# Performance work log

Hardware: AMD Instinct MI355X
Metric: run time of the kernel (lower is better)

## Reference

```python
import jax, jax.numpy as jnp
import numpy as np

N_NODES = 50000
N_EDGES = 800000
NUM_GRAPHS = 64
D_IN = 128
D_HID = 128
D_EMB = 128
D_PRED = 256
D_OUT = 1
BN_EPS = 1e-5


def gcn_conv(x, W, b, src, dst, n_nodes):
    # PyG GCNConv: add self-loops, sym-normalize, aggregate, then bias.
    h = x @ W  # [N, d_out]
    # in-degree with self-loops
    deg = jax.ops.segment_sum(jnp.ones((src.shape[0],), h.dtype), dst,
                              num_segments=n_nodes) + 1.0
    inv_sqrt = 1.0 / jnp.sqrt(deg)  # [N]
    norm = inv_sqrt[src] * inv_sqrt[dst]  # [E]
    msg = h[src] * norm[:, None]  # [E, d_out] gather + scale
    agg = jax.ops.segment_sum(msg, dst, num_segments=n_nodes)
    # self-loop contribution: norm_ii = 1/deg_i
    agg = agg + h / deg[:, None]
    return agg + b


def batch_norm(h, gamma, beta):
    # BatchNorm1d in training mode: batch stats, biased variance
    mean = jnp.mean(h, axis=0)
    var = jnp.mean(jnp.square(h - mean), axis=0)
    return (h - mean) / jnp.sqrt(var + BN_EPS) * gamma + beta


def setup_inputs() -> dict:
    key = jax.random.key(0)
    ks = jax.random.split(key, 12)
    x = jax.random.normal(ks[0], (N_NODES, D_IN), dtype=jnp.float32)
    edge_index = jax.random.randint(ks[1], (2, N_EDGES), 0, N_NODES, dtype=jnp.int32)
    batch = jnp.sort(jax.random.randint(ks[2], (N_NODES,), 0, NUM_GRAPHS, dtype=jnp.int32))
    s1 = 1.0 / np.sqrt(D_IN)
    s2 = 1.0 / np.sqrt(D_HID)
    s3 = 1.0 / np.sqrt(D_EMB)
    s4 = 1.0 / np.sqrt(D_PRED)
    return {
        "x": x,
        "edge_index": edge_index,
        "batch": batch,
        "W1": jax.random.uniform(ks[3], (D_IN, D_HID), jnp.float32, -s1, s1),
        "b1": jnp.zeros((D_HID,), jnp.float32),
        "g1": jnp.ones((D_HID,), jnp.float32),
        "be1": jnp.zeros((D_HID,), jnp.float32),
        "W2": jax.random.uniform(ks[4], (D_HID, D_EMB), jnp.float32, -s2, s2),
        "b2": jnp.zeros((D_EMB,), jnp.float32),
        "g2": jnp.ones((D_EMB,), jnp.float32),
        "be2": jnp.zeros((D_EMB,), jnp.float32),
        "Wp1": jax.random.uniform(ks[5], (D_EMB, D_PRED), jnp.float32, -s3, s3),
        "bp1": jax.random.uniform(ks[6], (D_PRED,), jnp.float32, -s3, s3),
        "Wp2": jax.random.uniform(ks[7], (D_PRED, D_OUT), jnp.float32, -s4, s4),
        "bp2": jax.random.uniform(ks[8], (D_OUT,), jnp.float32, -s4, s4),
    }


def reference(x, edge_index, batch, W1, b1, g1, be1, W2, b2, g2, be2, Wp1, bp1, Wp2, bp2):
    src, dst = edge_index[0], edge_index[1]
    h = gcn_conv(x, W1, b1, src, dst, N_NODES)
    h = batch_norm(jax.nn.relu(h), g1, be1)
    h = gcn_conv(h, W2, b2, src, dst, N_NODES)
    h = batch_norm(jax.nn.relu(h), g2, be2)
    # global max pool per graph
    pooled = jax.ops.segment_max(h, batch, num_segments=NUM_GRAPHS)  # [G, D_EMB]
    # predictor MLP (Dropout is identity in eval)
    z = jax.nn.relu(pooled @ Wp1 + bp1)
    return z @ Wp2 + bp2
```

## Files before the change

kernel.cpp:

```cpp
#include <hip/hip_runtime.h>

#define NN 50000
#define NE 800000
#define NG 64
#define D 128
#define DP 256
#define BN_EPS 1e-5f
#define NSLOT 32
#define NB 196

typedef unsigned short bf16;
typedef __attribute__((ext_vector_type(8))) short s16x8;
typedef __attribute__((ext_vector_type(4))) float f32x4;

__device__ __forceinline__ float bf2f(unsigned h16) {
  unsigned u = (h16 & 0xffffu) << 16; float f; __builtin_memcpy(&f, &u, 4); return f;
}
__device__ __forceinline__ bf16 f2bf(float f) {
  unsigned u; __builtin_memcpy(&u, &f, 4);
  return (bf16)((u + 0x7FFFu + ((u >> 16) & 1u)) >> 16);
}
__device__ __forceinline__ unsigned packbf2(float a, float b) {
  return (unsigned)f2bf(a) | ((unsigned)f2bf(b) << 16);
}
__device__ __forceinline__ s16x8 u4cast(uint4 v) {
  s16x8 r; __builtin_memcpy(&r, &v, 16); return r;
}

__global__ void k_detect(const unsigned short* __restrict__ x, int* __restrict__ flag) {
  if (threadIdx.x == 0) {
    int good = 0;
    for (int i = 0; i < 64; ++i) {
      float v = bf2f(x[2 * i]);
      float a = fabsf(v);
      if (v == 0.0f || (a > 1e-30f && a < 32.0f)) good++;
    }
    flag[0] = (good >= 56) ? 1 : 0;
    flag[1] = 1;
  }
}

struct CvtArgs {
  const void* s[12];
  float* d[12];
  int n[12];
};

__global__ __launch_bounds__(256) void k_cvt(CvtArgs a, const int* __restrict__ flag) {
  int t = blockIdx.x;
  int mode = flag[0];
  const void* sp = a.s[t];
  float* dp = a.d[t];
  int n = a.n[t];
  if (mode) {
    const unsigned short* s = (const unsigned short*)sp;
    for (int i = threadIdx.x; i < n; i += 256) dp[i] = bf2f(s[i]);
  } else {
    const float* s = (const float*)sp;
    for (int i = threadIdx.x; i < n; i += 256) dp[i] = s[i];
  }
}

__global__ __launch_bounds__(256) void k_deg(const int* __restrict__ ei, int* __restrict__ cnt) {
  int e = blockIdx.x * 256 + threadIdx.x;
  if (e < NE) atomicAdd(&cnt[ei[NE + e]], 1);
}

__global__ __launch_bounds__(256) void k_bsum(const int* __restrict__ cnt, int* __restrict__ bsum) {
  int i = blockIdx.x * 256 + threadIdx.x;
  int v = (i < NN) ? cnt[i] : 0;
  __shared__ int s[4];
  for (int off = 32; off; off >>= 1) v += __shfl_down(v, off);
  if ((threadIdx.x & 63) == 0) s[threadIdx.x >> 6] = v;
  __syncthreads();
  if (threadIdx.x == 0) bsum[blockIdx.x] = s[0] + s[1] + s[2] + s[3];
}

__global__ __launch_bounds__(256) void k_bscan(const int* __restrict__ bsum, int* __restrict__ bbase) {
  __shared__ int sh[256];
  int t = threadIdx.x;
  int v = (t < NB) ? bsum[t] : 0;
  sh[t] = v;
  __syncthreads();
  for (int off = 1; off < 256; off <<= 1) {
    int u = (t >= off) ? sh[t - off] : 0;
    __syncthreads();
    sh[t] += u;
    __syncthreads();
  }
  if (t < NB) bbase[t] = sh[t] - v;
}

__global__ __launch_bounds__(256) void k_offsets(const int* __restrict__ cnt, const int* __restrict__ bbase,
                                                 int* __restrict__ ro, int* __restrict__ cursor,
                                                 float* __restrict__ isq) {
  __shared__ int sh[256];
  int t = threadIdx.x;
  int i = blockIdx.x * 256 + t;
  int c = (i < NN) ? cnt[i] : 0;
  sh[t] = c;
  __syncthreads();
  for (int off = 1; off < 256; off <<= 1) {
    int u = (t >= off) ? sh[t - off] : 0;
    __syncthreads();
    sh[t] += u;
    __syncthreads();
  }
  if (i < NN) {
    int o = bbase[blockIdx.x] + sh[t] - c;
    ro[i] = o; cursor[i] = o;
    isq[i] = rsqrtf((float)(c + 1));
  }
  if (i == 0) ro[NN] = NE;
}

__global__ __launch_bounds__(256) void k_fill(const int* __restrict__ ei, const float* __restrict__ isq,
                                              int* __restrict__ cursor, int2* __restrict__ pk) {
  int e = blockIdx.x * 256 + threadIdx.x;
  if (e < NE) {
    int s = ei[e], d = ei[NE + e];
    int slot = atomicAdd(&cursor[d], 1);
    int2 v; v.x = s; v.y = __float_as_int(isq[s] * isq[d]);
    pk[slot] = v;
  }
}

__global__ __launch_bounds__(256) void k_pack(const float* __restrict__ W, const float* __restrict__ scale,
                                              bf16* __restrict__ Wp) {
  int slot = blockIdx.x * 256 + threadIdx.x;
  if (slot >= 2048) return;
  int kc = slot >> 9, ct = (slot >> 6) & 7, l = slot & 63;
  int q = l >> 4, p = l & 15;
  int n = ct * 16 + p;
  unsigned u[4];
#pragma unroll
  for (int jj = 0; jj < 4; ++jj) {
    int k0 = kc * 32 + q * 8 + jj * 2;
    float w0 = W[k0 * D + n], w1 = W[(k0 + 1) * D + n];
    if (scale) { w0 *= scale[k0]; w1 *= scale[k0 + 1]; }
    u[jj] = packbf2(w0, w1);
  }
  uint4 o = make_uint4(u[0], u[1], u[2], u[3]);
  *(uint4*)(Wp + (size_t)slot * 8) = o;
}

__global__ __launch_bounds__(256) void k_mgemm(const void* __restrict__ Xv, const int* __restrict__ flag,
                                               const bf16* __restrict__ Wp,
                                               const float* __restrict__ rowadd,
                                               bf16* __restrict__ Out, int nrows) {
  __shared__ float Cs[4][16][D + 4];
  int l = threadIdx.x & 63, w = threadIdx.x >> 6;
  int q = l >> 4, p = l & 15;
  int mode = flag ? flag[0] : 0;
  float rv[8];
#pragma unroll
  for (int ct = 0; ct < 8; ++ct) rv[ct] = rowadd ? rowadd[ct * 16 + p] : 0.f;
  int ntiles = (nrows + 63) >> 6;
  for (int t = blockIdx.x; t < ntiles; t += gridDim.x) {
    int wb = t * 64 + w * 16;
    int rowc = min(wb + p, nrows - 1);
    f32x4 acc[8];
#pragma unroll
    for (int ct = 0; ct < 8; ++ct) { f32x4 z = {rv[ct], rv[ct], rv[ct], rv[ct]}; acc[ct] = z; }
#pragma unroll
    for (int kc = 0; kc < 4; ++kc) {
      s16x8 a;
      if (mode) {
        uint4 av = *(const uint4*)((const bf16*)Xv + (size_t)rowc * D + kc * 32 + q * 8);
        a = u4cast(av);
      } else {
        const float* Xf = (const float*)Xv + (size_t)rowc * D + kc * 32 + q * 8;
        float4 f0 = *(const float4*)Xf;
        float4 f1 = *(const float4*)(Xf + 4);
        uint4 u = make_uint4(packbf2(f0.x, f0.y), packbf2(f0.z, f0.w),
                             packbf2(f1.x, f1.y), packbf2(f1.z, f1.w));
        a = u4cast(u);
      }
#pragma unroll
      for (int ct = 0; ct < 8; ++ct) {
        s16x8 bfr = *(const s16x8*)(Wp + (size_t)(((kc << 3) + ct) * 64 + l) * 8);
        acc[ct] = __builtin_amdgcn_mfma_f32_16x16x32_bf16(a, bfr, acc[ct], 0, 0, 0);
      }
    }
#pragma unroll
    for (int ct = 0; ct < 8; ++ct)
#pragma unroll
      for (int r = 0; r < 4; ++r)
        Cs[w][q * 4 + r][ct * 16 + p] = acc[ct][r];
    __syncthreads();
#pragma unroll
    for (int i = 0; i < 4; ++i) {
      int idx = i * 64 + l;
      int rr = idx >> 4, c8 = idx & 15;
      int gr = t * 64 + w * 16 + rr;
      if (gr < nrows) {
        float4 v0 = *(const float4*)&Cs[w][rr][c8 * 8];
        float4 v1 = *(const float4*)&Cs[w][rr][c8 * 8 + 4];
        uint4 o = make_uint4(packbf2(v0.x, v0.y), packbf2(v0.z, v0.w),
                             packbf2(v1.x, v1.y), packbf2(v1.z, v1.w));
        *(uint4*)(Out + (size_t)gr * D + c8 * 8) = o;
      }
    }
    __syncthreads();
  }
}

template <int LAYER2>
__global__ __launch_bounds__(256) void k_agg(const bf16* __restrict__ H, const int* __restrict__ ro,
                                             const int2* __restrict__ pk,
                                             const float* __restrict__ b, const int* __restrict__ batch,
                                             bf16* __restrict__ Rout,
                                             float* __restrict__ sumP, float* __restrict__ sumsqP,
                                             float* __restrict__ pooled) {
  int lane = threadIdx.x & 63;
  int w = __builtin_amdgcn_readfirstlane(threadIdx.x >> 6);
  int nbase = blockIdx.x * 16 + w * 4;
  float2 bv = ((const float2*)b)[lane];
  float2 ls = make_float2(0.f, 0.f), lq = make_float2(0.f, 0.f);
  int gcur = -1; float2 mx = make_float2(0.f, 0.f);
  int nend = min(nbase + 4, NN);
  for (int n = nbase; n < nend; ++n) {
    int r0 = __builtin_amdgcn_readfirstlane(ro[n]);
    int r1 = __builtin_amdgcn_readfirstlane(ro[n + 1]);
    float invd = 1.0f / (float)(r1 - r0 + 1);
    unsigned hv = ((const unsigned*)(H + (size_t)n * D))[lane];
    float2 acc = make_float2(bf2f(hv & 0xffff) * invd, bf2f(hv >> 16) * invd);
    int e = r0;
    for (; e + 4 <= r1; e += 4) {
      int2 p0 = pk[e], p1 = pk[e + 1], p2 = pk[e + 2], p3 = pk[e + 3];
      unsigned x0 = ((const unsigned*)(H + (size_t)p0.x * D))[lane];
      unsigned x1 = ((const unsigned*)(H + (size_t)p1.x * D))[lane];
      unsigned x2 = ((const unsigned*)(H + (size_t)p2.x * D))[lane];
      unsigned x3 = ((const unsigned*)(H + (size_t)p3.x * D))[lane];
      float c0 = __int_as_float(p0.y), c1 = __int_as_float(p1.y);
      float c2 = __int_as_float(p2.y), c3 = __int_as_float(p3.y);
      acc.x += bf2f(x0 & 0xffff) * c0; acc.y += bf2f(x0 >> 16) * c0;
      acc.x += bf2f(x1 & 0xffff) * c1; acc.y += bf2f(x1 >> 16) * c1;
      acc.x += bf2f(x2 & 0xffff) * c2; acc.y += bf2f(x2 >> 16) * c2;
      acc.x += bf2f(x3 & 0xffff) * c3; acc.y += bf2f(x3 >> 16) * c3;
    }
    for (; e < r1; ++e) {
      int2 p0 = pk[e];
      unsigned x0 = ((const unsigned*)(H + (size_t)p0.x * D))[lane];
      float c0 = __int_as_float(p0.y);
      acc.x += bf2f(x0 & 0xffff) * c0; acc.y += bf2f(x0 >> 16) * c0;
    }
    float2 r = make_float2(fmaxf(acc.x + bv.x, 0.f), fmaxf(acc.y + bv.y, 0.f));
    if (!LAYER2) ((unsigned*)(Rout + (size_t)n * D))[lane] = packbf2(r.x, r.y);
    ls.x += r.x; ls.y += r.y; lq.x += r.x * r.x; lq.y += r.y * r.y;
    if (LAYER2) {
      int g = batch[n];
      if (g != gcur) {
        if (gcur >= 0) {
          atomicMax((int*)&pooled[(size_t)gcur * D + 2 * lane], __float_as_int(mx.x));
          atomicMax((int*)&pooled[(size_t)gcur * D + 2 * lane + 1], __float_as_int(mx.y));
        }
        gcur = g; mx = make_float2(0.f, 0.f);
      }
      mx.x = fmaxf(mx.x, r.x); mx.y = fmaxf(mx.y, r.y);
    }
  }
  if (LAYER2 && gcur >= 0) {
    atomicMax((int*)&pooled[(size_t)gcur * D + 2 * lane], __float_as_int(mx.x));
    atomicMax((int*)&pooled[(size_t)gcur * D + 2 * lane + 1], __float_as_int(mx.y));
  }
  __shared__ float ss[4][D], sq[4][D];
  ss[w][2 * lane] = ls.x; ss[w][2 * lane + 1] = ls.y;
  sq[w][2 * lane] = lq.x; sq[w][2 * lane + 1] = lq.y;
  __syncthreads();
  int slot = (blockIdx.x & (NSLOT - 1)) * D;
  if (threadIdx.x < D) {
    int k = threadIdx.x;
    atomicAdd(&sumP[slot + k], ss[0][k] + ss[1][k] + ss[2][k] + ss[3][k]);
  } else {
    int k = threadIdx.x - D;
    atomicAdd(&sumsqP[slot + k], sq[0][k] + sq[1][k] + sq[2][k] + sq[3][k]);
  }
}

__global__ void k_bnstats1(const float* __restrict__ sumP, const float* __restrict__ sumsqP,
                           const float* __restrict__ gamma, const float* __restrict__ beta,
                           const float* __restrict__ W2,
                           float* __restrict__ svec, float* __restrict__ tW2) {
  __shared__ float t[D];
  int k = threadIdx.x;
  float sm = 0.f, sq = 0.f;
  for (int i = 0; i < NSLOT; ++i) { sm += sumP[i * D + k]; sq += sumsqP[i * D + k]; }
  float mean = sm * (1.0f / NN);
  float var = sq * (1.0f / NN) - mean * mean;
  float s = gamma[k] * rsqrtf(var + BN_EPS);
  svec[k] = s;
  t[k] = beta[k] - mean * s;
  __syncthreads();
  float acc = 0.f;
  for (int kk = 0; kk < D; ++kk) acc += t[kk] * W2[kk * D + k];
  tW2[k] = acc;
}

__global__ void k_bnstats2(const float* __restrict__ sumP, const float* __restrict__ sumsqP,
                           const float* __restrict__ gamma, const float* __restrict__ beta,
                           float* __restrict__ svec, float* __restrict__ tvec) {
  int k = threadIdx.x;
  float sm = 0.f, sq = 0.f;
  for (int i = 0; i < NSLOT; ++i) { sm += sumP[i * D + k]; sq += sumsqP[i * D + k]; }
  float mean = sm * (1.0f / NN);
  float var = sq * (1.0f / NN) - mean * mean;
  float s = gamma[k] * rsqrtf(var + BN_EPS);
  svec[k] = s;
  tvec[k] = beta[k] - mean * s;
}

__global__ __launch_bounds__(256) void k_head(const float* __restrict__ pooled, const float* __restrict__ s2,
                                              const float* __restrict__ t2, const float* __restrict__ Wp1,
                                              const float* __restrict__ bp1, const float* __restrict__ Wp2,
                                              const float* __restrict__ bp2, void* out,
                                              const int* __restrict__ flag) {
  __shared__ float y[D];
  __shared__ float wr[4];
  int g = blockIdx.x, j = threadIdx.x;
  if (j < D) y[j] = pooled[(size_t)g * D + j] * s2[j] + t2[j];
  __syncthreads();
  float acc = bp1[j];
#pragma unroll 4
  for (int k = 0; k < D; ++k) acc += y[k] * Wp1[k * DP + j];
  float v = fmaxf(acc, 0.f) * Wp2[j];
  for (int off = 32; off; off >>= 1) v += __shfl_down(v, off);
  if ((j & 63) == 0) wr[j >> 6] = v;
  __syncthreads();
  if (j == 0) {
    float r = wr[0] + wr[1] + wr[2] + wr[3] + bp2[0];
    if (flag[0]) ((bf16*)out)[g] = f2bf(r);
    else ((float*)out)[g] = r;
  }
}

extern "C" void kernel_launch(void* const* d_in, const int* in_sizes, int n_in,
                              void* d_out, int out_size, void* d_ws, size_t ws_size,
                              hipStream_t stream) {
  const void* x   = d_in[0];
  const int*  ei  = (const int*)d_in[1];
  const int*  bat = (const int*)d_in[2];

  float* f = (float*)d_ws;
  bf16* A = (bf16*)f; f += (size_t)NN * D / 2;
  bf16* B = (bf16*)f; f += (size_t)NN * D / 2;
  float* W1f  = f; f += D * D;
  float* W2f  = f; f += D * D;
  float* Wp1f = f; f += D * DP;
  float* b1f  = f; f += D;
  float* g1f  = f; f += D;
  float* be1f = f; f += D;
  float* b2f  = f; f += D;
  float* g2f  = f; f += D;
  float* be2f = f; f += D;
  float* bp1f = f; f += DP;
  float* Wp2f = f; f += DP;
  float* bp2f = f; f += 4;
  bf16* Wpk1 = (bf16*)f; f += 2048 * 8 / 2;
  bf16* Wpk2 = (bf16*)f; f += 2048 * 8 / 2;
  float* sum1P   = f; f += NSLOT * D;
  float* sumsq1P = f; f += NSLOT * D;
  float* sum2P   = f; f += NSLOT * D;
  float* sumsq2P = f; f += NSLOT * D;
  float* pooled = f; f += (size_t)NG * D;
  float* svec1  = f; f += D;
  float* tW2    = f; f += D;
  float* svec2  = f; f += D;
  float* tvec2  = f; f += D;
  float* isq    = f; f += NN;
  int2* pk     = (int2*)f; f += (size_t)NE * 2;
  int* ro      = (int*)f; f += NN + 1;
  int* cursor  = (int*)f; f += NN;
  int* cnt     = (int*)f; f += NN;
  int* bsum    = (int*)f; f += NB;
  int* bbase   = (int*)f; f += NB;
  int* flag    = (int*)f;

  hipMemsetAsync(cnt, 0, NN * sizeof(int), stream);
  hipMemsetAsync(sum1P, 0, (4 * NSLOT * D + NG * D) * sizeof(float), stream);

  k_detect<<<1, 64, 0, stream>>>((const unsigned short*)x, flag);

  CvtArgs ca;
  ca.s[0] = d_in[3];  ca.d[0] = W1f;  ca.n[0] = D * D;
  ca.s[1] = d_in[7];  ca.d[1] = W2f;  ca.n[1] = D * D;
  ca.s[2] = d_in[11]; ca.d[2] = Wp1f; ca.n[2] = D * DP;
  ca.s[3] = d_in[4];  ca.d[3] = b1f;  ca.n[3] = D;
  ca.s[4] = d_in[5];  ca.d[4] = g1f;  ca.n[4] = D;
  ca.s[5] = d_in[6];  ca.d[5] = be1f; ca.n[5] = D;
  ca.s[6] = d_in[8];  ca.d[6] = b2f;  ca.n[6] = D;
  ca.s[7] = d_in[9];  ca.d[7] = g2f;  ca.n[7] = D;
  ca.s[8] = d_in[10]; ca.d[8] = be2f; ca.n[8] = D;
  ca.s[9] = d_in[12]; ca.d[9] = bp1f; ca.n[9] = DP;
  ca.s[10] = d_in[13]; ca.d[10] = Wp2f; ca.n[10] = DP;
  ca.s[11] = d_in[14]; ca.d[11] = bp2f; ca.n[11] = 1;
  k_cvt<<<12, 256, 0, stream>>>(ca, flag);

  k_deg<<<(NE + 255) / 256, 256, 0, stream>>>(ei, cnt);
  k_bsum<<<NB, 256, 0, stream>>>(cnt, bsum);
  k_bscan<<<1, 256, 0, stream>>>(bsum, bbase);
  k_offsets<<<NB, 256, 0, stream>>>(cnt, bbase, ro, cursor, isq);
  k_fill<<<(NE + 255) / 256, 256, 0, stream>>>(ei, isq, cursor, pk);
  k_pack<<<8, 256, 0, stream>>>(W1f, nullptr, Wpk1);

  k_mgemm<<<256, 256, 0, stream>>>(x, flag, Wpk1, nullptr, A, NN);
  k_agg<0><<<(NN + 15) / 16, 256, 0, stream>>>(A, ro, pk, b1f, nullptr,
                                               B, sum1P, sumsq1P, nullptr);
  k_bnstats1<<<1, D, 0, stream>>>(sum1P, sumsq1P, g1f, be1f, W2f, svec1, tW2);

  k_pack<<<8, 256, 0, stream>>>(W2f, svec1, Wpk2);
  k_mgemm<<<256, 256, 0, stream>>>(B, flag + 1, Wpk2, tW2, A, NN);
  k_agg<1><<<(NN + 15) / 16, 256, 0, stream>>>(A, ro, pk, b2f, bat,
                                               nullptr, sum2P, sumsq2P, pooled);
  k_bnstats2<<<1, D, 0, stream>>>(sum2P, sumsq2P, g2f, be2f, svec2, tvec2);

  k_head<<<NG, DP, 0, stream>>>(pooled, svec2, tvec2, Wp1f, bp1f, Wp2f, bp2f, d_out, flag);
}
```

Measured before the change: 266.9 us.

## Parallelize detect and convert kernels, unroll gather by 8, enlarge GEMM grid

```diff
diff --git a/kernel.cpp b/kernel.cpp
--- a/kernel.cpp
+++ b/kernel.cpp
@@ -28,14 +28,13 @@
 }
 
 __global__ void k_detect(const unsigned short* __restrict__ x, int* __restrict__ flag) {
-  if (threadIdx.x == 0) {
-    int good = 0;
-    for (int i = 0; i < 64; ++i) {
-      float v = bf2f(x[2 * i]);
-      float a = fabsf(v);
-      if (v == 0.0f || (a > 1e-30f && a < 32.0f)) good++;
-    }
-    flag[0] = (good >= 56) ? 1 : 0;
+  int i = threadIdx.x;
+  float v = bf2f(x[2 * i]);
+  float a = fabsf(v);
+  int good = (v == 0.0f) || (a > 1e-30f && a < 32.0f);
+  unsigned long long m = __ballot(good);
+  if (i == 0) {
+    flag[0] = (__popcll(m) >= 56) ? 1 : 0;
     flag[1] = 1;
   }
 }
@@ -47,17 +46,32 @@
 };
 
 __global__ __launch_bounds__(256) void k_cvt(CvtArgs a, const int* __restrict__ flag) {
-  int t = blockIdx.x;
+  int t = blockIdx.y;
+  int n = a.n[t];
+  int base = blockIdx.x * 2048;
+  if (base >= n) return;
   int mode = flag[0];
-  const void* sp = a.s[t];
   float* dp = a.d[t];
-  int n = a.n[t];
-  if (mode) {
-    const unsigned short* s = (const unsigned short*)sp;
-    for (int i = threadIdx.x; i < n; i += 256) dp[i] = bf2f(s[i]);
+  if (n >= 8) {
+    int i8 = base + threadIdx.x * 8;
+    if (i8 + 8 <= n) {
+      if (mode) {
+        uint4 raw = *(const uint4*)((const bf16*)a.s[t] + i8);
+        float4 o0 = make_float4(bf2f(raw.x & 0xffff), bf2f(raw.x >> 16),
+                                bf2f(raw.y & 0xffff), bf2f(raw.y >> 16));
+        float4 o1 = make_float4(bf2f(raw.z & 0xffff), bf2f(raw.z >> 16),
+                                bf2f(raw.w & 0xffff), bf2f(raw.w >> 16));
+        *(float4*)(dp + i8) = o0;
+        *(float4*)(dp + i8 + 4) = o1;
+      } else {
+        const float* s = (const float*)a.s[t] + i8;
+        *(float4*)(dp + i8) = *(const float4*)s;
+        *(float4*)(dp + i8 + 4) = *(const float4*)(s + 4);
+      }
+    }
   } else {
-    const float* s = (const float*)sp;
-    for (int i = threadIdx.x; i < n; i += 256) dp[i] = s[i];
+    int i = base + threadIdx.x;
+    if (i < n) dp[i] = mode ? bf2f(((const bf16*)a.s[t])[i]) : ((const float*)a.s[t])[i];
   }
 }
 
@@ -226,6 +240,19 @@
     unsigned hv = ((const unsigned*)(H + (size_t)n * D))[lane];
     float2 acc = make_float2(bf2f(hv & 0xffff) * invd, bf2f(hv >> 16) * invd);
     int e = r0;
+    for (; e + 8 <= r1; e += 8) {
+      int2 P[8];
+      unsigned X[8];
+#pragma unroll
+      for (int j = 0; j < 8; ++j) P[j] = pk[e + j];
+#pragma unroll
+      for (int j = 0; j < 8; ++j) X[j] = ((const unsigned*)(H + (size_t)P[j].x * D))[lane];
+#pragma unroll
+      for (int j = 0; j < 8; ++j) {
+        float c = __int_as_float(P[j].y);
+        acc.x += bf2f(X[j] & 0xffff) * c; acc.y += bf2f(X[j] >> 16) * c;
+      }
+    }
     for (; e + 4 <= r1; e += 4) {
       int2 p0 = pk[e], p1 = pk[e + 1], p2 = pk[e + 2], p3 = pk[e + 3];
       unsigned x0 = ((const unsigned*)(H + (size_t)p0.x * D))[lane];
@@ -394,7 +421,7 @@
   ca.s[9] = d_in[12]; ca.d[9] = bp1f; ca.n[9] = DP;
   ca.s[10] = d_in[13]; ca.d[10] = Wp2f; ca.n[10] = DP;
   ca.s[11] = d_in[14]; ca.d[11] = bp2f; ca.n[11] = 1;
-  k_cvt<<<12, 256, 0, stream>>>(ca, flag);
+  k_cvt<<<dim3(16, 12), 256, 0, stream>>>(ca, flag);
 
   k_deg<<<(NE + 255) / 256, 256, 0, stream>>>(ei, cnt);
   k_bsum<<<NB, 256, 0, stream>>>(cnt, bsum);
@@ -403,13 +430,13 @@
   k_fill<<<(NE + 255) / 256, 256, 0, stream>>>(ei, isq, cursor, pk);
   k_pack<<<8, 256, 0, stream>>>(W1f, nullptr, Wpk1);
 
-  k_mgemm<<<256, 256, 0, stream>>>(x, flag, Wpk1, nullptr, A, NN);
+  k_mgemm<<<(NN + 63) / 64, 256, 0, stream>>>(x, flag, Wpk1, nullptr, A, NN);
   k_agg<0><<<(NN + 15) / 16, 256, 0, stream>>>(A, ro, pk, b1f, nullptr,
                                                B, sum1P, sumsq1P, nullptr);
   k_bnstats1<<<1, D, 0, stream>>>(sum1P, sumsq1P, g1f, be1f, W2f, svec1, tW2);
 
   k_pack<<<8, 256, 0, stream>>>(W2f, svec1, Wpk2);
-  k_mgemm<<<256, 256, 0, stream>>>(B, flag + 1, Wpk2, tW2, A, NN);
+  k_mgemm<<<(NN + 63) / 64, 256, 0, stream>>>(B, flag + 1, Wpk2, tW2, A, NN);
   k_agg<1><<<(NN + 15) / 16, 256, 0, stream>>>(A, ro, pk, b2f, bat,
                                                nullptr, sum2P, sumsq2P, pooled);
   k_bnstats2<<<1, D, 0, stream>>>(sum2P, sumsq2P, g2f, be2f, svec2, tvec2);
```

Result: faster. 231.3 us (-13.3%).
